# Performance work log

Hardware: AMD Instinct MI355X
Metric: run time of the kernel (lower is better)

Reference implementation:

```python
import jax, jax.numpy as jnp
import numpy as np

# CTBG circuit dims: units=[512,512,512], action_sz=6
UNIT1, UNIT2, UNIT3, ACTION = 512, 512, 512, 6
D_GPE_IN = UNIT1 * 3          # 1536  (striatum D1/D2/D3 blocks)
D_GPE_OUT = UNIT2 * 3         # 1536
D_GPI_IN = (UNIT1 + UNIT2) * 3  # 3072 (striatum + GPe/STN blocks)
D_GPI_OUT = UNIT2 * 3         # 1536
B = 16384


def setup_inputs() -> dict:
    key = jax.random.key(0)
    ks = jax.random.split(key, 12)
    x = jax.random.normal(ks[0], (B, D_GPE_IN), jnp.float32)
    # per-unit diagonal connectivity masks (unit_diags): [units, input_dim]
    gpe_mask = jax.random.bernoulli(ks[1], 0.5, (D_GPE_OUT, D_GPE_IN)).astype(jnp.float32)
    gpi_mask = jax.random.bernoulli(ks[2], 0.5, (D_GPI_OUT, D_GPI_IN)).astype(jnp.float32)
    # non-negative weights, uniform [0, 0.01) as in the TF initializer
    gpe_w = jax.random.uniform(ks[3], (D_GPE_IN, D_GPE_OUT), jnp.float32, 0.0, 0.01)
    gpe_b = jnp.zeros((D_GPE_OUT,), jnp.float32)
    gpi_w = jax.random.uniform(ks[4], (D_GPI_IN, D_GPI_OUT), jnp.float32, 0.0, 0.01)
    gpi_b = jnp.zeros((D_GPI_OUT,), jnp.float32)
    # Motor_cortex dense stack
    w1 = jax.random.normal(ks[5], (D_GPI_OUT, UNIT3), jnp.float32) / np.sqrt(D_GPI_OUT)
    b1 = jnp.zeros((UNIT3,), jnp.float32)
    w2 = jax.random.normal(ks[6], (UNIT3, UNIT3), jnp.float32) / np.sqrt(UNIT3)
    b2 = jnp.zeros((UNIT3,), jnp.float32)
    w3 = jax.random.normal(ks[7], (UNIT3, ACTION), jnp.float32) / np.sqrt(UNIT3)
    b3 = jnp.zeros((ACTION,), jnp.float32)
    return {"x": x, "gpe_mask": gpe_mask, "gpe_w": gpe_w, "gpe_b": gpe_b,
            "gpi_mask": gpi_mask, "gpi_w": gpi_w, "gpi_b": gpi_b,
            "w1": w1, "b1": b1, "w2": w2, "b2": b2, "w3": w3, "b3": b3}


def _masked_layer(x, mask, w, b):
    # TF original: p = transpose(matmul(diag(mask_u), x^T)) -> [B,U,I];
    #              f = diag_part(matmul(p, w)) + b
    # algebraically: f[b,u] = sum_i mask[u,i] * x[b,i] * w[i,u] + b[u]
    # which is a plain matmul against the element-wise masked weight.
    return x @ (w * mask.T) + b


def reference(x, gpe_mask, gpe_w, gpe_b, gpi_mask, gpi_w, gpi_b,
              w1, b1, w2, b2, w3, b3):
    gpe_out = _masked_layer(x, gpe_mask, gpe_w, gpe_b)          # [B, 1536]
    gpi_in = jnp.concatenate([x, gpe_out], axis=-1)              # [B, 3072]
    gpi_out = _masked_layer(gpi_in, gpi_mask, gpi_w, gpi_b)      # [B, 1536]
    h = jax.nn.relu(gpi_out @ w1 + b1)
    h = jax.nn.relu(h @ w2 + b2)
    return jax.nn.relu(h @ w3 + b3)                              # [B, 6]
```

## Files before the change

kernel.cpp:

```cpp
#include <hip/hip_runtime.h>
#include <stdint.h>


typedef __attribute__((ext_vector_type(8))) short short8;
typedef __attribute__((ext_vector_type(4))) float floatx4;

typedef const __attribute__((address_space(1))) void* gas1_cvp;
typedef __attribute__((address_space(3))) void* gas3_vp;

__device__ __forceinline__ void load_lds16(const void* g, void* s) {
    __builtin_amdgcn_global_load_lds((gas1_cvp)g, (gas3_vp)s, 16, 0, 0);
}

__device__ __forceinline__ unsigned short f2bf(float f) {
    unsigned int u = __float_as_uint(f);
    u = u + 0x7fffu + ((u >> 16) & 1u);
    return (unsigned short)(u >> 16);
}
__device__ __forceinline__ float bf2f(unsigned short h) {
    return __uint_as_float(((unsigned int)h) << 16);
}
__device__ __forceinline__ short8 cvt8(float4 a, float4 b) {
    short8 r;
    r[0] = (short)f2bf(a.x); r[1] = (short)f2bf(a.y);
    r[2] = (short)f2bf(a.z); r[3] = (short)f2bf(a.w);
    r[4] = (short)f2bf(b.x); r[5] = (short)f2bf(b.y);
    r[6] = (short)f2bf(b.z); r[7] = (short)f2bf(b.w);
    return r;
}

__device__ __forceinline__ void dev_prep_t(
        float (*tile)[65],
        const float* __restrict__ w, const float* __restrict__ mask,
        unsigned short* __restrict__ out,
        int ldw, int ldm, int ldo, int bx, int by) {
    int n0 = bx * 64;
    int k0 = by * 64;
    int t = threadIdx.x;
    int c4 = (t & 15) * 4;
    int r  = t >> 4;

    #pragma unroll
    for (int p = 0; p < 4; ++p) {
        int kk = r + p * 16;
        float4 v = *(const float4*)(w + (size_t)(k0 + kk) * ldw + n0 + c4);
        tile[c4 + 0][kk] = v.x;
        tile[c4 + 1][kk] = v.y;
        tile[c4 + 2][kk] = v.z;
        tile[c4 + 3][kk] = v.w;
    }
    __syncthreads();
    #pragma unroll
    for (int p = 0; p < 4; ++p) {
        int nn = r + p * 16;
        float mx = 1.f, my = 1.f, mz = 1.f, mw = 1.f;
        if (mask) {
            float4 m = *(const float4*)(mask + (size_t)(n0 + nn) * ldm + k0 + c4);
            mx = m.x; my = m.y; mz = m.z; mw = m.w;
        }
        ushort4 o;
        o.x = f2bf(tile[nn][c4 + 0] * mx);
        o.y = f2bf(tile[nn][c4 + 1] * my);
        o.z = f2bf(tile[nn][c4 + 2] * mz);
        o.w = f2bf(tile[nn][c4 + 3] * mw);
        *(ushort4*)(out + (size_t)(n0 + nn) * ldo + k0 + c4) = o;
    }
}

__device__ __forceinline__ void dev_prep_nt(
        float (*tile)[65],
        const float* __restrict__ w, const float* __restrict__ mask,
        unsigned short* __restrict__ out,
        int ldw, int ldm, int ldo, int bx, int by) {
    int j0 = bx * 64;
    int i0 = by * 64;
    int t = threadIdx.x;
    int c4 = (t & 15) * 4;
    int r  = t >> 4;

    #pragma unroll
    for (int p = 0; p < 4; ++p) {
        int jj = r + p * 16;
        float4 m = *(const float4*)(mask + (size_t)(j0 + jj) * ldm + i0 + c4);
        tile[c4 + 0][jj] = m.x;
        tile[c4 + 1][jj] = m.y;
        tile[c4 + 2][jj] = m.z;
        tile[c4 + 3][jj] = m.w;
    }
    __syncthreads();
    #pragma unroll
    for (int p = 0; p < 4; ++p) {
        int ii = r + p * 16;
        float4 v = *(const float4*)(w + (size_t)(i0 + ii) * ldw + j0 + c4);
        ushort4 o;
        o.x = f2bf(v.x * tile[ii][c4 + 0]);
        o.y = f2bf(v.y * tile[ii][c4 + 1]);
        o.z = f2bf(v.z * tile[ii][c4 + 2]);
        o.w = f2bf(v.w * tile[ii][c4 + 3]);
        *(ushort4*)(out + (size_t)(i0 + ii) * ldo + j0 + c4) = o;
    }
}

__global__ __launch_bounds__(256) void prep_all_kernel(
        const float* __restrict__ gpe_w, const float* __restrict__ gpe_mask,
        const float* __restrict__ gpi_w, const float* __restrict__ gpi_mask,
        const float* __restrict__ w1, const float* __restrict__ w2,
        unsigned short* __restrict__ wi_topnt, unsigned short* __restrict__ wibot_ui,
        unsigned short* __restrict__ we_nt, unsigned short* __restrict__ w1t,
        unsigned short* __restrict__ w2t, float* __restrict__ zero_base) {
    __shared__ float tile[64][65];
    int b = blockIdx.x;
    if (b < 576) {
        dev_prep_nt(tile, gpi_w, gpi_mask, wi_topnt, 1536, 3072, 1536,
                    b % 24, b / 24);
    } else if (b < 1152) {
        int lb = b - 576;
        dev_prep_nt(tile, gpi_w + (size_t)1536 * 1536, gpi_mask + 1536, wibot_ui,
                    1536, 3072, 1536, lb % 24, lb / 24);
    } else if (b < 1728) {
        int lb = b - 1152;
        dev_prep_nt(tile, gpe_w, gpe_mask, we_nt, 1536, 1536, 1536,
                    lb % 24, lb / 24);
    } else if (b < 1920) {
        int lb = b - 1728;
        dev_prep_t(tile, w1, nullptr, w1t, 512, 0, 1536, lb % 8, lb / 8);
    } else if (b < 1984) {
        int lb = b - 1920;
        dev_prep_t(tile, w2, nullptr, w2t, 512, 0, 512, lb % 8, lb / 8);
    } else {
        float4 z = {0.f, 0.f, 0.f, 0.f};
        float* p = zero_base + (size_t)(b - 1984) * 4096 + threadIdx.x * 16;
        #pragma unroll
        for (int i = 0; i < 4; ++i) *(float4*)(p + i * 4) = z;
    }
}

template <bool F32A>
__device__ __forceinline__ void dev_combine_splitk(
        unsigned short* As, unsigned short* Bs,
        const void* __restrict__ Aop,
        const unsigned short* __restrict__ B,
        float* __restrict__ C,
        int kbase, int ntl, int bx, int by) {
    const int m0 = by * 64;
    const int n0 = bx * 128;
    const int t    = threadIdx.x;
    const int lane = t & 63;
    const int w    = t >> 6;
    const int wm   = w >> 1;
    const int wn   = w & 1;
    const int lm   = lane & 15;
    const int lq   = lane >> 4;

    const int srow = lane >> 2;
    const int scol = (lane & 3) * 8;

    size_t aidx[2];
    int rbA[2], awr[2];
    #pragma unroll
    for (int i = 0; i < 2; ++i) {
        aidx[i] = (size_t)(m0 + w * 16 + srow) * 1536 + i * 32 + scol + kbase;
        rbA[i]  = i * 2048 + w * 512;
        awr[i]  = i * 2048 + (w * 16 + srow) * 32 + scol;
    }
    size_t bidx[4];
    int rbB[4];
    #pragma unroll
    for (int i = 0; i < 4; ++i) {
        int rows = w * 32 + (i >> 1) * 16;
        bidx[i] = (size_t)(n0 + rows + srow) * 1536 + (i & 1) * 32 + scol + kbase;
        rbB[i]  = (i & 1) * 4096 + rows * 32;
    }

    int aro[2][2], bro[2][4];
    #pragma unroll
    for (int ks = 0; ks < 2; ++ks) {
        #pragma unroll
        for (int mi = 0; mi < 2; ++mi)
            aro[ks][mi] = ks * 2048 + (wm * 32 + mi * 16 + lm) * 32 + lq * 8;
        #pragma unroll
        for (int ni = 0; ni < 4; ++ni)
            bro[ks][ni] = ks * 4096 + (wn * 64 + ni * 16 + lm) * 32 + lq * 8;
    }

    const float* Af = (const float*)Aop;
    const unsigned short* Ab = (const unsigned short*)Aop;

    floatx4 acc[2][4] = {};
    float4 ra[2][2];

    #pragma unroll
    for (int i = 0; i < 4; ++i) load_lds16(B + bidx[i], Bs + rbB[i]);
    if (F32A) {
        #pragma unroll
        for (int i = 0; i < 2; ++i) {
            ra[i][0] = *(const float4*)(Af + aidx[i]);
            ra[i][1] = *(const float4*)(Af + aidx[i] + 4);
        }
        #pragma unroll
        for (int i = 0; i < 2; ++i)
            *(short8*)(As + awr[i]) = cvt8(ra[i][0], ra[i][1]);
    } else {
        #pragma unroll
        for (int i = 0; i < 2; ++i) load_lds16(Ab + aidx[i], As + rbA[i]);
    }
    __syncthreads();

    int buf = 0;
    for (int tt = 0; tt < ntl; ++tt) {
        const int kn = (tt + 1) << 6;
        const int more = tt + 1 < ntl;
        if (more) {
            const int nbA = (buf ^ 1) * 4096;
            const int nbB = (buf ^ 1) * 8192;
            #pragma unroll
            for (int i = 0; i < 4; ++i)
                load_lds16(B + bidx[i] + kn, Bs + nbB + rbB[i]);
            if (F32A) {
                #pragma unroll
                for (int i = 0; i < 2; ++i) {
                    ra[i][0] = *(const float4*)(Af + aidx[i] + kn);
                    ra[i][1] = *(const float4*)(Af + aidx[i] + kn + 4);
                }
            } else {
                #pragma unroll
                for (int i = 0; i < 2; ++i)
                    load_lds16(Ab + aidx[i] + kn, As + nbA + rbA[i]);
            }
        }
        const int cA = buf * 4096, cB = buf * 8192;
        #pragma unroll
        for (int ks = 0; ks < 2; ++ks) {
            short8 af[2], bf8[4];
            #pragma unroll
            for (int mi = 0; mi < 2; ++mi)
                af[mi] = *(const short8*)(As + cA + aro[ks][mi]);
            #pragma unroll
            for (int ni = 0; ni < 4; ++ni)
                bf8[ni] = *(const short8*)(Bs + cB + bro[ks][ni]);
            #pragma unroll
            for (int mi = 0; mi < 2; ++mi)
                #pragma unroll
                for (int ni = 0; ni < 4; ++ni)
                    acc[mi][ni] = __builtin_amdgcn_mfma_f32_16x16x32_bf16(
                        af[mi], bf8[ni], acc[mi][ni], 0, 0, 0);
        }
        if (more) {
            if (F32A) {
                const int nbA = (buf ^ 1) * 4096;
                #pragma unroll
                for (int i = 0; i < 2; ++i)
                    *(short8*)(As + nbA + awr[i]) = cvt8(ra[i][0], ra[i][1]);
            }
            __syncthreads();
        }
        buf ^= 1;
    }

    #pragma unroll
    for (int mi = 0; mi < 2; ++mi) {
        int rbase = m0 + wm * 32 + mi * 16 + lq * 4;
        #pragma unroll
        for (int ni = 0; ni < 4; ++ni) {
            int cc = n0 + wn * 64 + ni * 16 + lm;
            #pragma unroll
            for (int r = 0; r < 4; ++r)
                unsafeAtomicAdd(&C[(size_t)(rbase + r) * 1536 + cc],
                                acc[mi][ni][r]);
        }
    }
}

__global__ __launch_bounds__(256) void combineA_kernel(
        const unsigned short* __restrict__ w1t,
        const unsigned short* __restrict__ wibot_ui,
        float* __restrict__ t1f) {
    __shared__ unsigned short As[2 * 4096];
    __shared__ unsigned short Bs[2 * 8192];
    int b = blockIdx.x;
    int s = b / 96;
    int r = b % 96;
    dev_combine_splitk<false>(As, Bs, w1t, wibot_ui, t1f,
                              s * 512, 8, r % 12, r / 12);
}

__global__ __launch_bounds__(256) void combineB_kernel(
        const unsigned short* __restrict__ w1t,
        const unsigned short* __restrict__ wi_topnt,
        const float* __restrict__ t1f,
        const unsigned short* __restrict__ we_nt,
        float* __restrict__ w1cf) {
    __shared__ unsigned short As[2 * 4096];
    __shared__ unsigned short Bs[2 * 8192];
    int b = blockIdx.x;
    int c = b / 96;
    int r = b % 96;
    int kbase = (c % 3) * 512;
    if (c < 3) {
        dev_combine_splitk<false>(As, Bs, w1t, wi_topnt, w1cf,
                                  kbase, 8, r % 12, r / 12);
    } else {
        dev_combine_splitk<true>(As, Bs, t1f, we_nt, w1cf,
                                 kbase, 8, r % 12, r / 12);
    }
}

__global__ __launch_bounds__(256) void finalize_kernel(
        const float* __restrict__ w1cf, unsigned short* __restrict__ w1ct,
        const unsigned short* __restrict__ w1t, const float* __restrict__ t1f,
        const float* __restrict__ gpi_b, const float* __restrict__ gpe_b,
        const float* __restrict__ b1, float* __restrict__ b1c) {
    int b = blockIdx.x;
    if (b < 384) {
        size_t base = (size_t)b * 2048 + threadIdx.x * 8;
        float4 v0 = *(const float4*)(w1cf + base);
        float4 v1 = *(const float4*)(w1cf + base + 4);
        ushort4 o0, o1;
        o0.x = f2bf(v0.x); o0.y = f2bf(v0.y); o0.z = f2bf(v0.z); o0.w = f2bf(v0.w);
        o1.x = f2bf(v1.x); o1.y = f2bf(v1.y); o1.z = f2bf(v1.z); o1.w = f2bf(v1.w);
        *(ushort4*)(w1ct + base) = o0;
        *(ushort4*)(w1ct + base + 4) = o1;
    } else {
        int n = (b - 384) * 4 + (threadIdx.x >> 6);
        int lane = threadIdx.x & 63;
        const unsigned short* r1 = w1t + (size_t)n * 1536;
        const float* r2 = t1f + (size_t)n * 1536;
        float s = 0.f;
        for (int i = lane; i < 1536; i += 64)
            s += gpi_b[i] * bf2f(r1[i]) + gpe_b[i] * r2[i];
        #pragma unroll
        for (int off = 32; off; off >>= 1) s += __shfl_down(s, off, 64);
        if (lane == 0) b1c[n] = b1[n] + s;
    }
}

__global__ __launch_bounds__(256) void gemm_a32_kernel(
        const float* __restrict__ A,
        const unsigned short* __restrict__ Bt,
        const float* __restrict__ bias,
        unsigned short* __restrict__ C,
        int K, int lda, int ldc) {
    __shared__ unsigned short As[2 * 8192];
    __shared__ unsigned short Bs[2 * 8192];

    const int bid = blockIdx.x;
    const int loc = bid >> 3;
    const int m0 = ((bid & 7) * 16 + (loc >> 2)) * 128;
    const int n0 = (loc & 3) * 128;

    const int t    = threadIdx.x;
    const int lane = t & 63;
    const int w    = t >> 6;
    const int wm   = w >> 1;
    const int wn   = w & 1;
    const int lm   = lane & 15;
    const int lq   = lane >> 4;

    const int srow = lane >> 2;
    const int scol = (lane & 3) * 8;

    const float* ag[4];
    const unsigned short* bg[4];
    int rb[4];
    int awr[4];
    #pragma unroll
    for (int i = 0; i < 4; ++i) {
        int rows = w * 32 + (i >> 1) * 16;
        ag[i]  = A  + (size_t)(m0 + rows + srow) * lda + (i & 1) * 32 + scol;
        bg[i]  = Bt + (size_t)(n0 + rows + srow) * K   + (i & 1) * 32 + scol;
        rb[i]  = (i & 1) * 4096 + rows * 32;
        awr[i] = (i & 1) * 4096 + (rows + srow) * 32 + scol;
    }

    int aro[2][4], bro[2][4];
    #pragma unroll
    for (int ks = 0; ks < 2; ++ks)
        #pragma unroll
        for (int i = 0; i < 4; ++i) {
            aro[ks][i] = ks * 4096 + (wm * 64 + i * 16 + lm) * 32 + lq * 8;
            bro[ks][i] = ks * 4096 + (wn * 64 + i * 16 + lm) * 32 + lq * 8;
        }

    floatx4 acc[4][4] = {};
    float4 ra[4][2];

    #pragma unroll
    for (int i = 0; i < 4; ++i) load_lds16(bg[i], Bs + rb[i]);
    #pragma unroll
    for (int i = 0; i < 4; ++i) {
        ra[i][0] = *(const float4*)(ag[i]);
        ra[i][1] = *(const float4*)(ag[i] + 4);
    }
    #pragma unroll
    for (int i = 0; i < 4; ++i)
        *(short8*)(As + awr[i]) = cvt8(ra[i][0], ra[i][1]);
    __syncthreads();

    const int nt = K >> 6;
    int buf = 0;
    for (int tt = 0; tt < nt; ++tt) {
        const int kn = (tt + 1) << 6;
        const int more = kn < K;
        if (more) {
            const int nb = (buf ^ 1) * 8192;
            #pragma unroll
            for (int i = 0; i < 4; ++i)
                load_lds16(bg[i] + kn, Bs + nb + rb[i]);
            #pragma unroll
            for (int i = 0; i < 4; ++i) {
                ra[i][0] = *(const float4*)(ag[i] + kn);
                ra[i][1] = *(const float4*)(ag[i] + kn + 4);
            }
        }
        const int cb = buf * 8192;
        #pragma unroll
        for (int ks = 0; ks < 2; ++ks) {
            short8 af[4], bf8[4];
            #pragma unroll
            for (int i = 0; i < 4; ++i) {
                af[i]  = *(const short8*)(As + cb + aro[ks][i]);
                bf8[i] = *(const short8*)(Bs + cb + bro[ks][i]);
            }
            #pragma unroll
            for (int mi = 0; mi < 4; ++mi)
                #pragma unroll
                for (int ni = 0; ni < 4; ++ni)
                    acc[mi][ni] = __builtin_amdgcn_mfma_f32_16x16x32_bf16(
                        af[mi], bf8[ni], acc[mi][ni], 0, 0, 0);
        }
        if (more) {
            const int nb = (buf ^ 1) * 8192;
            #pragma unroll
            for (int i = 0; i < 4; ++i)
                *(short8*)(As + nb + awr[i]) = cvt8(ra[i][0], ra[i][1]);
            __syncthreads();
        }
        buf ^= 1;
    }

    float bv[4];
    #pragma unroll
    for (int ni = 0; ni < 4; ++ni) bv[ni] = bias[n0 + wn * 64 + ni * 16 + lm];

    #pragma unroll
    for (int mi = 0; mi < 4; ++mi) {
        int rbase = m0 + wm * 64 + mi * 16 + lq * 4;
        #pragma unroll
        for (int ni = 0; ni < 4; ++ni) {
            int cc = n0 + wn * 64 + ni * 16 + lm;
            #pragma unroll
            for (int r = 0; r < 4; ++r) {
                float v = fmaxf(acc[mi][ni][r] + bv[ni], 0.f);
                C[(size_t)(rbase + r) * ldc + cc] = f2bf(v);
            }
        }
    }
}

__global__ __launch_bounds__(256) void gemm_bt_kernel(
        const unsigned short* __restrict__ A,
        const unsigned short* __restrict__ Bt,
        const float* __restrict__ bias,
        unsigned short* __restrict__ C,
        int K, int lda, int ldc) {
    __shared__ unsigned short As[2 * 8192];
    __shared__ unsigned short Bs[2 * 8192];

    const int bid = blockIdx.x;
    const int loc = bid >> 3;
    const int m0 = ((bid & 7) * 16 + (loc >> 2)) * 128;
    const int n0 = (loc & 3) * 128;

    const int t    = threadIdx.x;
    const int lane = t & 63;
    const int w    = t >> 6;
    const int wm   = w >> 1;
    const int wn   = w & 1;
    const int lm   = lane & 15;
    const int lq   = lane >> 4;

    const int srow = lane >> 2;
    const int scol = (lane & 3) * 8;

    const unsigned short* ag[4];
    const unsigned short* bg[4];
    int rb[4];
    #pragma unroll
    for (int i = 0; i < 4; ++i) {
        int rows = w * 32 + (i >> 1) * 16;
        ag[i] = A  + (size_t)(m0 + rows + srow) * lda + (i & 1) * 32 + scol;
        bg[i] = Bt + (size_t)(n0 + rows + srow) * K   + (i & 1) * 32 + scol;
        rb[i] = (i & 1) * 4096 + rows * 32;
    }

    int aro[2][4], bro[2][4];
    #pragma unroll
    for (int ks = 0; ks < 2; ++ks)
        #pragma unroll
        for (int i = 0; i < 4; ++i) {
            aro[ks][i] = ks * 4096 + (wm * 64 + i * 16 + lm) * 32 + lq * 8;
            bro[ks][i] = ks * 4096 + (wn * 64 + i * 16 + lm) * 32 + lq * 8;
        }

    floatx4 acc[4][4] = {};

    #pragma unroll
    for (int i = 0; i < 4; ++i) {
        load_lds16(ag[i], As + rb[i]);
        load_lds16(bg[i], Bs + rb[i]);
    }
    __syncthreads();

    const int nt = K >> 6;
    int buf = 0;
    for (int tt = 0; tt < nt; ++tt) {
        const int kn = (tt + 1) << 6;
        const int more = kn < K;
        if (more) {
            const int nb = (buf ^ 1) * 8192;
            #pragma unroll
            for (int i = 0; i < 4; ++i) {
                load_lds16(ag[i] + kn, As + nb + rb[i]);
                load_lds16(bg[i] + kn, Bs + nb + rb[i]);
            }
        }
        const int cb = buf * 8192;
        #pragma unroll
        for (int ks = 0; ks < 2; ++ks) {
            short8 af[4], bf8[4];
            #pragma unroll
            for (int i = 0; i < 4; ++i) {
                af[i]  = *(const short8*)(As + cb + aro[ks][i]);
                bf8[i] = *(const short8*)(Bs + cb + bro[ks][i]);
            }
            #pragma unroll
            for (int mi = 0; mi < 4; ++mi)
                #pragma unroll
                for (int ni = 0; ni < 4; ++ni)
                    acc[mi][ni] = __builtin_amdgcn_mfma_f32_16x16x32_bf16(
                        af[mi], bf8[ni], acc[mi][ni], 0, 0, 0);
        }
        if (more) __syncthreads();
        buf ^= 1;
    }

    float bv[4];
    #pragma unroll
    for (int ni = 0; ni < 4; ++ni) bv[ni] = bias[n0 + wn * 64 + ni * 16 + lm];

    #pragma unroll
    for (int mi = 0; mi < 4; ++mi) {
        int rbase = m0 + wm * 64 + mi * 16 + lq * 4;
        #pragma unroll
        for (int ni = 0; ni < 4; ++ni) {
            int cc = n0 + wn * 64 + ni * 16 + lm;
            #pragma unroll
            for (int r = 0; r < 4; ++r) {
                float v = fmaxf(acc[mi][ni][r] + bv[ni], 0.f);
                C[(size_t)(rbase + r) * ldc + cc] = f2bf(v);
            }
        }
    }
}

__global__ void head_kernel(const unsigned short* __restrict__ h,
                            const float* __restrict__ w3,
                            const float* __restrict__ b3,
                            float* __restrict__ out) {
    int row = blockIdx.x * 4 + (threadIdx.x >> 6);
    int lane = threadIdx.x & 63;
    const unsigned short* hp = h + (size_t)row * 512 + lane * 8;
    ushort4 ha = *(const ushort4*)(hp);
    ushort4 hb = *(const ushort4*)(hp + 4);
    float hv[8] = {bf2f(ha.x), bf2f(ha.y), bf2f(ha.z), bf2f(ha.w),
                   bf2f(hb.x), bf2f(hb.y), bf2f(hb.z), bf2f(hb.w)};
    const float* wp = w3 + lane * 48;
    float s[6] = {0.f, 0.f, 0.f, 0.f, 0.f, 0.f};
    #pragma unroll
    for (int j = 0; j < 8; ++j)
        #pragma unroll
        for (int a = 0; a < 6; ++a)
            s[a] += hv[j] * wp[j * 6 + a];
    #pragma unroll
    for (int a = 0; a < 6; ++a)
        #pragma unroll
        for (int off = 32; off; off >>= 1)
            s[a] += __shfl_down(s[a], off, 64);
    if (lane == 0) {
        #pragma unroll
        for (int a = 0; a < 6; ++a)
            out[(size_t)row * 6 + a] = fmaxf(s[a] + b3[a], 0.f);
    }
}

extern "C" void kernel_launch(void* const* d_in, const int* in_sizes, int n_in,
                              void* d_out, int out_size, void* d_ws, size_t ws_size,
                              hipStream_t stream) {
    const float* x        = (const float*)d_in[0];
    const float* gpe_mask = (const float*)d_in[1];
    const float* gpe_w    = (const float*)d_in[2];
    const float* gpe_b    = (const float*)d_in[3];
    const float* gpi_mask = (const float*)d_in[4];
    const float* gpi_w    = (const float*)d_in[5];
    const float* gpi_b    = (const float*)d_in[6];
    const float* w1       = (const float*)d_in[7];
    const float* b1       = (const float*)d_in[8];
    const float* w2       = (const float*)d_in[9];
    const float* b2       = (const float*)d_in[10];
    const float* w3       = (const float*)d_in[11];
    const float* b3       = (const float*)d_in[12];
    float* out = (float*)d_out;

    char* ws = (char*)d_ws;
    unsigned short* h1        = (unsigned short*)(ws);
    unsigned short* h2        = (unsigned short*)(ws + 16777216);
    float*          t1f       = (float*)(ws + 16777216);
    float*          w1cf      = (float*)(ws + 19922944);
    unsigned short* wi_topnt  = (unsigned short*)(ws + 33554432);
    unsigned short* wibot_ui  = (unsigned short*)(ws + 38273024);
    unsigned short* we_nt     = (unsigned short*)(ws + 42991616);
    unsigned short* w1t       = (unsigned short*)(ws + 47710208);
    unsigned short* w2t       = (unsigned short*)(ws + 49283072);
    unsigned short* w1ct      = (unsigned short*)(ws + 49807360);
    float*          b1c       = (float*)(ws + 51380224);

    prep_all_kernel<<<dim3(2368), dim3(256), 0, stream>>>(
        gpe_w, gpe_mask, gpi_w, gpi_mask, w1, w2,
        wi_topnt, wibot_ui, we_nt, w1t, w2t, t1f);

    combineA_kernel<<<dim3(288), dim3(256), 0, stream>>>(w1t, wibot_ui, t1f);

    combineB_kernel<<<dim3(576), dim3(256), 0, stream>>>(
        w1t, wi_topnt, t1f, we_nt, w1cf);

    finalize_kernel<<<dim3(512), dim3(256), 0, stream>>>(
        w1cf, w1ct, w1t, t1f, gpi_b, gpe_b, b1, b1c);

    gemm_a32_kernel<<<dim3(512), dim3(256), 0, stream>>>(
        x, w1ct, b1c, h1, 1536, 1536, 512);
    gemm_bt_kernel<<<dim3(512), dim3(256), 0, stream>>>(
        h1, w2t, b2, h2, 512, 512, 512);
    head_kernel<<<dim3(16384 / 4), dim3(256), 0, stream>>>(h2, w3, b3, out);
}
```

Before: 322.4 us.

## Deepen fp32-A prefetch pipeline in gemm_a32 with manual waitcnt and unrolled double buffers

Restructures the fp32-input GEMM main loop to unroll by two with fixed LDS buffers, prefetching A register tiles two K-steps ahead (ra/rx) while B streams directly to LDS one step ahead. Replaces __syncthreads with explicit vmcnt/lgkmcnt waits and s_barrier so outstanding A loads can remain in flight across barriers, and adds sched_barriers to pin instruction order. Also sets launch_bounds occupancy hint of 2 blocks per CU. The extra register buffers raise VGPR pressure, and the loop assumes an even tile count, with the hand-coded vmcnt relying on exact load counts.

```diff
diff --git a/kernel.cpp b/kernel.cpp
--- a/kernel.cpp
+++ b/kernel.cpp
@@ -334,7 +334,7 @@
     }
 }
 
-__global__ __launch_bounds__(256) void gemm_a32_kernel(
+__global__ __launch_bounds__(256, 2) void gemm_a32_kernel(
         const float* __restrict__ A,
         const unsigned short* __restrict__ Bt,
         const float* __restrict__ bias,
@@ -382,60 +382,102 @@
         }
 
     floatx4 acc[4][4] = {};
-    float4 ra[4][2];
+    float4 ra[4][2], rx[4][2];
+
+    auto compute = [&](int cb) {
+        #pragma unroll
+        for (int ks = 0; ks < 2; ++ks) {
+            short8 af[4], bf8[4];
+            #pragma unroll
+            for (int i = 0; i < 4; ++i) {
+                af[i]  = *(const short8*)(As + cb + aro[ks][i]);
+                bf8[i] = *(const short8*)(Bs + cb + bro[ks][i]);
+            }
+            #pragma unroll
+            for (int mi = 0; mi < 4; ++mi)
+                #pragma unroll
+                for (int ni = 0; ni < 4; ++ni)
+                    acc[mi][ni] = __builtin_amdgcn_mfma_f32_16x16x32_bf16(
+                        af[mi], bf8[ni], acc[mi][ni], 0, 0, 0);
+        }
+    };
 
     #pragma unroll
     for (int i = 0; i < 4; ++i) load_lds16(bg[i], Bs + rb[i]);
+    __builtin_amdgcn_sched_barrier(0);
     #pragma unroll
     for (int i = 0; i < 4; ++i) {
         ra[i][0] = *(const float4*)(ag[i]);
         ra[i][1] = *(const float4*)(ag[i] + 4);
     }
     #pragma unroll
+    for (int i = 0; i < 4; ++i) {
+        rx[i][0] = *(const float4*)(ag[i] + 64);
+        rx[i][1] = *(const float4*)(ag[i] + 68);
+    }
+    #pragma unroll
     for (int i = 0; i < 4; ++i)
         *(short8*)(As + awr[i]) = cvt8(ra[i][0], ra[i][1]);
-    __syncthreads();
+    asm volatile("s_waitcnt lgkmcnt(0)" ::: "memory");
+    __builtin_amdgcn_s_barrier();
 
     const int nt = K >> 6;
-    int buf = 0;
-    for (int tt = 0; tt < nt; ++tt) {
-        const int kn = (tt + 1) << 6;
-        const int more = kn < K;
-        if (more) {
-            const int nb = (buf ^ 1) * 8192;
+    for (int tt = 0; tt < nt; tt += 2) {
+        {
+            const int kb = (tt + 1) << 6;
             #pragma unroll
             for (int i = 0; i < 4; ++i)
-                load_lds16(bg[i] + kn, Bs + nb + rb[i]);
-            #pragma unroll
-            for (int i = 0; i < 4; ++i) {
-                ra[i][0] = *(const float4*)(ag[i] + kn);
-                ra[i][1] = *(const float4*)(ag[i] + kn + 4);
-            }
-        }
-        const int cb = buf * 8192;
-        #pragma unroll
-        for (int ks = 0; ks < 2; ++ks) {
-            short8 af[4], bf8[4];
-            #pragma unroll
-            for (int i = 0; i < 4; ++i) {
-                af[i]  = *(const short8*)(As + cb + aro[ks][i]);
-                bf8[i] = *(const short8*)(Bs + cb + bro[ks][i]);
-            }
-            #pragma unroll
-            for (int mi = 0; mi < 4; ++mi)
-                #pragma unroll
-                for (int ni = 0; ni < 4; ++ni)
-                    acc[mi][ni] = __builtin_amdgcn_mfma_f32_16x16x32_bf16(
-                        af[mi], bf8[ni], acc[mi][ni], 0, 0, 0);
-        }
-        if (more) {
-            const int nb = (buf ^ 1) * 8192;
+                load_lds16(bg[i] + kb, Bs + 8192 + rb[i]);
+            __builtin_amdgcn_sched_barrier(0);
+            const bool ld2 = (tt + 2) < nt;
+            if (ld2) {
+                const int ka = (tt + 2) << 6;
+                #pragma unroll
+                for (int i = 0; i < 4; ++i) {
+                    ra[i][0] = *(const float4*)(ag[i] + ka);
+                    ra[i][1] = *(const float4*)(ag[i] + ka + 4);
+                }
+            }
+            __builtin_amdgcn_sched_barrier(0);
+            compute(0);
             #pragma unroll
             for (int i = 0; i < 4; ++i)
-                *(short8*)(As + nb + awr[i]) = cvt8(ra[i][0], ra[i][1]);
-            __syncthreads();
-        }
-        buf ^= 1;
+                *(short8*)(As + 8192 + awr[i]) = cvt8(rx[i][0], rx[i][1]);
+            if (ld2) asm volatile("s_waitcnt vmcnt(8)" ::: "memory");
+            else     asm volatile("s_waitcnt vmcnt(0)" ::: "memory");
+            asm volatile("s_waitcnt lgkmcnt(0)" ::: "memory");
+            __builtin_amdgcn_s_barrier();
+        }
+        {
+            const bool mb = (tt + 2) < nt;
+            if (mb) {
+                const int kb = (tt + 2) << 6;
+                #pragma unroll
+                for (int i = 0; i < 4; ++i)
+                    load_lds16(bg[i] + kb, Bs + rb[i]);
+            }
+            __builtin_amdgcn_sched_barrier(0);
+            const bool ld3 = (tt + 3) < nt;
+            if (ld3) {
+                const int ka = (tt + 3) << 6;
+                #pragma unroll
+                for (int i = 0; i < 4; ++i) {
+                    rx[i][0] = *(const float4*)(ag[i] + ka);
+                    rx[i][1] = *(const float4*)(ag[i] + ka + 4);
+                }
+            }
+            __builtin_amdgcn_sched_barrier(0);
+            compute(8192);
+            if (mb) {
+                #pragma unroll
+                for (int i = 0; i < 4; ++i)
+                    *(short8*)(As + awr[i]) = cvt8(ra[i][0], ra[i][1]);
+                if (ld3) asm volatile("s_waitcnt vmcnt(8)" ::: "memory");
+                else     asm volatile("s_waitcnt vmcnt(0)" ::: "memory");
+                asm volatile("s_waitcnt lgkmcnt(0)" ::: "memory");
+                __builtin_amdgcn_s_barrier();
+            }
+        }
     }
 
     float bv[4];
```

New measurement: 319.1 us. No clear change (-1.0%).
